# Performance work log

Hardware: AMD Instinct MI355X
Metric: run time of the kernel (lower is better)

## Reference

```python
import jax, jax.numpy as jnp
import numpy as np

B = 16384
K = 30
LAYERS = 3 * K          # 90
V_LEN = 2 * K           # 60
Z_LEN = 8 * K           # 240
IN_LEN = 3 * K + V_LEN  # 150


def setup_inputs() -> dict:
    key = jax.random.key(0)
    ks = jax.random.split(key, 9)
    Hr = jax.random.normal(ks[0], (B, K), dtype=jnp.float32)
    HH = jax.random.normal(ks[1], (B, K, K), dtype=jnp.float32)
    std = 0.01
    W1 = std * jax.random.normal(ks[2], (LAYERS, Z_LEN, IN_LEN), dtype=jnp.float32)
    b1 = std * jax.random.normal(ks[3], (LAYERS, Z_LEN), dtype=jnp.float32)
    W2 = std * jax.random.normal(ks[4], (LAYERS, K, Z_LEN), dtype=jnp.float32)
    b2 = std * jax.random.normal(ks[5], (LAYERS, K), dtype=jnp.float32)
    W3 = std * jax.random.normal(ks[6], (LAYERS, V_LEN, Z_LEN), dtype=jnp.float32)
    b3 = std * jax.random.normal(ks[7], (LAYERS, V_LEN), dtype=jnp.float32)
    kappa = jax.random.uniform(ks[8], (LAYERS,), dtype=jnp.float32)  # torch.rand(1) per layer
    return {"Hr": Hr, "HH": HH, "W1": W1, "b1": b1, "W2": W2, "b2": b2,
            "W3": W3, "b3": b3, "kappa": kappa}


def reference(Hr, HH, W1, b1, W2, b2, W3, b3, kappa):
    b = Hr.shape[0]
    v0 = jnp.zeros((b, V_LEN), dtype=Hr.dtype)
    t0 = jnp.zeros((b, K), dtype=Hr.dtype)
    tt0 = jnp.zeros((b, K), dtype=Hr.dtype)

    def step(carry, params):
        v, t, t_tilde = carry
        w1, bb1, w2, bb2, w3, bb3, kap = params
        tH = jnp.einsum('bk,bkj->bj', t, HH)                  # [B,K]
        concat = jnp.concatenate([Hr, v, t, tH], axis=1)      # [B,150]
        z = jax.nn.relu(concat @ w1.T + bb1)                  # [B,240]
        t_tilde = t_tilde + z @ w2.T + bb2                    # [B,30]
        ak = jnp.abs(kap)
        t_new = -1.0 + jax.nn.relu(t_tilde + kap) / ak - jax.nn.relu(t_tilde - kap) / ak
        v = v + z @ w3.T + bb3                                # [B,60]
        return (v, t_new, t_tilde), t_new

    _, ts = jax.lax.scan(step, (v0, t0, tt0), (W1, b1, W2, b2, W3, b3, kappa))
    return ts  # [LAYERS, B, K] == t[1:] in torch code
```

## Files before the change

kernel.cpp:

```cpp
#include <hip/hip_runtime.h>

typedef unsigned short u16;
typedef float    f32x4  __attribute__((ext_vector_type(4)));
typedef _Float16 f16x8  __attribute__((ext_vector_type(8)));
typedef short    short8 __attribute__((ext_vector_type(8)));

#define BB 16384
#define KK 30
#define NLAYER 90
#define ROWS 64
#define NBLK (BB / ROWS)
#define THREADS 1024

#define NT1 16
#define KS1 5
#define NT2 6
#define KS2 8

#define SZ1  (NLAYER * NT1 * KS1 * 512)
#define SZ23 (NLAYER * NT2 * KS2 * 512)
#define WS_NEEDED ((size_t)4 * (SZ1 + SZ23) + (size_t)4 * (NLAYER * 256 + NLAYER * 96))

#define A_STRIDE 168
#define Z_STRIDE 264
#define TO_STRIDE 33

#define MFMA(a, b, c) __builtin_amdgcn_mfma_f32_16x16x32_f16((a), (b), (c), 0, 0, 0)

__device__ __forceinline__ void splitf(float x, u16& hi, u16& lo) {
    _Float16 h = (_Float16)x;
    _Float16 l = (_Float16)(x - (float)h);
    hi = __builtin_bit_cast(u16, h);
    lo = __builtin_bit_cast(u16, l);
}
__device__ __forceinline__ f16x8 ldfrag(const u16* p) {
    return __builtin_bit_cast(f16x8, *(const short8*)p);
}

__global__ void prep(const float* __restrict__ W1, const float* __restrict__ W2,
                     const float* __restrict__ W3, const float* __restrict__ b1,
                     const float* __restrict__ b2, const float* __restrict__ b3,
                     u16* __restrict__ W1Fhi, u16* __restrict__ W1Flo,
                     u16* __restrict__ W23Fhi, u16* __restrict__ W23Flo,
                     float* __restrict__ b1p, float* __restrict__ b23p)
{
    int idx = blockIdx.x * 256 + threadIdx.x;
    if (idx < SZ1) {
        int j = idx & 7, lane = (idx >> 3) & 63;
        int r = idx >> 9, ks = r % 5; r /= 5;
        int nt = r % 16, l = r / 16;
        int k = ks * 32 + (lane >> 4) * 8 + j;
        int n = nt * 16 + (lane & 15);
        float wv = (k < 150 && n < 240) ? W1[((size_t)l * 240 + n) * 150 + k] : 0.f;
        splitf(wv, W1Fhi[idx], W1Flo[idx]);
    }
    if (idx < SZ23) {
        int j = idx & 7, lane = (idx >> 3) & 63;
        int r = idx >> 9, ks = r % 8; r /= 8;
        int nt = r % 6, l = r / 6;
        int k = ks * 32 + (lane >> 4) * 8 + j;
        int n = nt * 16 + (lane & 15);
        float wv = 0.f;
        if (k < 240) {
            if (n < 30)      wv = W2[((size_t)l * 30 + n) * 240 + k];
            else if (n < 90) wv = W3[((size_t)l * 60 + (n - 30)) * 240 + k];
        }
        splitf(wv, W23Fhi[idx], W23Flo[idx]);
    }
    if (idx < NLAYER * 256) {
        int l = idx >> 8, c = idx & 255;
        b1p[idx] = (c < 240) ? b1[l * 240 + c] : 0.f;
    }
    if (idx < NLAYER * 96) {
        int l = idx / 96, c = idx % 96;
        b23p[idx] = (c < 30) ? b2[l * 30 + c] : (c < 90 ? b3[l * 60 + (c - 30)] : 0.f);
    }
}

__global__ __launch_bounds__(THREADS, 4)
void detnet_kernel(const float* __restrict__ Hr, const float* __restrict__ HH,
                   const float* __restrict__ kappa,
                   const u16* __restrict__ W1Fhi, const u16* __restrict__ W1Flo,
                   const u16* __restrict__ W23Fhi, const u16* __restrict__ W23Flo,
                   const float* __restrict__ b1p, const float* __restrict__ b23p,
                   float* __restrict__ out)
{
    __shared__ u16 aT_hi[ROWS][A_STRIDE], aT_lo[ROWS][A_STRIDE];
    __shared__ u16 zT_hi[ROWS][Z_STRIDE], zT_lo[ROWS][Z_STRIDE];
    __shared__ float tOut[ROWS][TO_STRIDE];

    const int tid  = threadIdx.x;
    const int b0   = blockIdx.x * ROWS;
    const int w    = tid >> 6;
    const int lane = tid & 63;
    const int h    = lane >> 4;
    const int q    = lane & 15;

    const int ra = tid >> 4;
    const int sa = tid & 15;
    float2 hreg[KK];
    if (sa < 15) {
        const float* hh = HH + (size_t)(b0 + ra) * (KK * KK) + 2 * sa;
        #pragma unroll
        for (int k = 0; k < KK; ++k) hreg[k] = *(const float2*)(hh + k * KK);
    } else {
        #pragma unroll
        for (int k = 0; k < KK; ++k) hreg[k] = make_float2(0.f, 0.f);
    }

    const int cnt = w >> 1;
    const int cmh = w & 1;
    float st[2][4];
    #pragma unroll
    for (int m = 0; m < 2; ++m)
        #pragma unroll
        for (int r = 0; r < 4; ++r) st[m][r] = 0.f;

    for (int i = tid; i < ROWS * A_STRIDE; i += THREADS) { (&aT_hi[0][0])[i] = 0; (&aT_lo[0][0])[i] = 0; }
    for (int i = tid; i < ROWS * Z_STRIDE; i += THREADS) { (&zT_hi[0][0])[i] = 0; (&zT_lo[0][0])[i] = 0; }
    for (int i = tid; i < ROWS * TO_STRIDE; i += THREADS) (&tOut[0][0])[i] = 0.f;
    __syncthreads();
    for (int i = tid; i < ROWS * KK; i += THREADS) {
        int r = i / KK, k = i - r * KK;
        splitf(Hr[(size_t)(b0 + r) * KK + k], aT_hi[r][k], aT_lo[r][k]);
    }
    __syncthreads();

    for (int l = 0; l < NLAYER; ++l) {
        if (l > 0 && tid < ROWS * KK / 4) {
            f32x4 o;
            int e = tid * 4;
            #pragma unroll
            for (int i = 0; i < 4; ++i) {
                int ee = e + i, r = ee / 30, k2 = ee - 30 * r;
                o[i] = tOut[r][k2];
            }
            __builtin_nontemporal_store(o, (f32x4*)(out + ((size_t)(l - 1) * BB + b0) * KK + e));
        }

        if (l > 0 && sa < 15) {
            float a0 = 0.f, a1 = 0.f;
            #pragma unroll
            for (int k = 0; k < KK; ++k) {
                float tk = tOut[ra][k];
                a0 += tk * hreg[k].x;
                a1 += tk * hreg[k].y;
            }
            u16 h0, l0, h1, l1;
            splitf(a0, h0, l0); splitf(a1, h1, l1);
            *(unsigned int*)&aT_hi[ra][120 + 2 * sa] = (unsigned int)h0 | ((unsigned int)h1 << 16);
            *(unsigned int*)&aT_lo[ra][120 + 2 * sa] = (unsigned int)l0 | ((unsigned int)l1 << 16);
        }
        __syncthreads();

        {
            f32x4 acc[4];
            {
                float bi = b1p[l * 256 + w * 16 + q];
                f32x4 bv = {bi, bi, bi, bi};
                #pragma unroll
                for (int m = 0; m < 4; ++m) acc[m] = bv;
            }
            #pragma unroll 2
            for (int ks = 0; ks < KS1; ++ks) {
                size_t off = ((((size_t)l * NT1 + w) * KS1 + ks) * 64 + lane) * 8;
                f16x8 bh = ldfrag(W1Fhi + off);
                f16x8 bl = ldfrag(W1Flo + off);
                #pragma unroll
                for (int m = 0; m < 4; ++m) {
                    f16x8 ah = ldfrag(&aT_hi[m * 16 + q][ks * 32 + h * 8]);
                    f16x8 al = ldfrag(&aT_lo[m * 16 + q][ks * 32 + h * 8]);
                    acc[m] = MFMA(ah, bh, acc[m]);
                    acc[m] = MFMA(ah, bl, acc[m]);
                    acc[m] = MFMA(al, bh, acc[m]);
                }
            }
            #pragma unroll
            for (int m = 0; m < 4; ++m) {
                int col = w * 16 + q;
                #pragma unroll
                for (int reg = 0; reg < 4; ++reg) {
                    int row = m * 16 + 4 * h + reg;
                    float zv = fmaxf(acc[m][reg], 0.f);
                    splitf(zv, zT_hi[row][col], zT_lo[row][col]);
                }
            }
        }
        __syncthreads();

        if (w < 12) {
            const float kap = kappa[l];
            const float inv = 1.0f / fabsf(kap);
            f32x4 acc[2];
            {
                float bi = b23p[l * 96 + cnt * 16 + q];
                f32x4 bv = {bi, bi, bi, bi};
                acc[0] = bv; acc[1] = bv;
            }
            #pragma unroll 2
            for (int ks = 0; ks < KS2; ++ks) {
                size_t off = ((((size_t)l * NT2 + cnt) * KS2 + ks) * 64 + lane) * 8;
                f16x8 bh = ldfrag(W23Fhi + off);
                f16x8 bl = ldfrag(W23Flo + off);
                #pragma unroll
                for (int mm = 0; mm < 2; ++mm) {
                    f16x8 ah = ldfrag(&zT_hi[(cmh * 2 + mm) * 16 + q][ks * 32 + h * 8]);
                    f16x8 al = ldfrag(&zT_lo[(cmh * 2 + mm) * 16 + q][ks * 32 + h * 8]);
                    acc[mm] = MFMA(ah, bh, acc[mm]);
                    acc[mm] = MFMA(ah, bl, acc[mm]);
                    acc[mm] = MFMA(al, bh, acc[mm]);
                }
            }
            const int col = cnt * 16 + q;
            const bool isT = col < 30;
            const bool isV = (col >= 30) & (col < 90);
            #pragma unroll
            for (int mm = 0; mm < 2; ++mm)
                #pragma unroll
                for (int reg = 0; reg < 4; ++reg) {
                    float s2 = st[mm][reg] + acc[mm][reg];
                    int row = (cmh * 2 + mm) * 16 + 4 * h + reg;
                    if (isT) {
                        st[mm][reg] = s2;
                        float tn = -1.0f + fmaxf(s2 + kap, 0.f) * inv - fmaxf(s2 - kap, 0.f) * inv;
                        tOut[row][col] = tn;
                        splitf(tn, aT_hi[row][90 + col], aT_lo[row][90 + col]);
                    } else if (isV) {
                        st[mm][reg] = s2;
                        splitf(s2, aT_hi[row][col], aT_lo[row][col]);
                    }
                }
        }
        __syncthreads();
    }

    if (tid < ROWS * KK / 4) {
        f32x4 o;
        int e = tid * 4;
        #pragma unroll
        for (int i = 0; i < 4; ++i) {
            int ee = e + i, r = ee / 30, k2 = ee - 30 * r;
            o[i] = tOut[r][k2];
        }
        __builtin_nontemporal_store(o, (f32x4*)(out + ((size_t)(NLAYER - 1) * BB + b0) * KK + e));
    }
}

extern "C" void kernel_launch(void* const* d_in, const int* in_sizes, int n_in,
                              void* d_out, int out_size, void* d_ws, size_t ws_size,
                              hipStream_t stream) {
    const float* Hr = (const float*)d_in[0];
    const float* HH = (const float*)d_in[1];
    const float* W1 = (const float*)d_in[2];
    const float* b1 = (const float*)d_in[3];
    const float* W2 = (const float*)d_in[4];
    const float* b2 = (const float*)d_in[5];
    const float* W3 = (const float*)d_in[6];
    const float* b3 = (const float*)d_in[7];
    const float* kp = (const float*)d_in[8];
    float* out = (float*)d_out;

    if (ws_size < WS_NEEDED) return;

    u16* W1Fhi  = (u16*)d_ws;
    u16* W1Flo  = W1Fhi + SZ1;
    u16* W23Fhi = W1Flo + SZ1;
    u16* W23Flo = W23Fhi + SZ23;
    float* b1p  = (float*)(W23Flo + SZ23);
    float* b23p = b1p + NLAYER * 256;

    prep<<<dim3((SZ1 + 255) / 256), dim3(256), 0, stream>>>(
        W1, W2, W3, b1, b2, b3, W1Fhi, W1Flo, W23Fhi, W23Flo, b1p, b23p);
    detnet_kernel<<<dim3(NBLK), dim3(THREADS), 0, stream>>>(
        Hr, HH, kp, W1Fhi, W1Flo, W23Fhi, W23Flo, b1p, b23p, out);
}
```

Baseline: 759.2 us.

## Use 32x32x16 MFMA tiles for the first-layer GEMM

```diff
diff --git a/kernel.cpp b/kernel.cpp
--- a/kernel.cpp
+++ b/kernel.cpp
@@ -2,6 +2,7 @@
 
 typedef unsigned short u16;
 typedef float    f32x4  __attribute__((ext_vector_type(4)));
+typedef float    f32x16 __attribute__((ext_vector_type(16)));
 typedef _Float16 f16x8  __attribute__((ext_vector_type(8)));
 typedef short    short8 __attribute__((ext_vector_type(8)));
 
@@ -12,8 +13,8 @@
 #define NBLK (BB / ROWS)
 #define THREADS 1024
 
-#define NT1 16
-#define KS1 5
+#define NT1 8
+#define KS1 10
 #define NT2 6
 #define KS2 8
 
@@ -25,7 +26,8 @@
 #define Z_STRIDE 264
 #define TO_STRIDE 33
 
-#define MFMA(a, b, c) __builtin_amdgcn_mfma_f32_16x16x32_f16((a), (b), (c), 0, 0, 0)
+#define MFMA16(a, b, c) __builtin_amdgcn_mfma_f32_16x16x32_f16((a), (b), (c), 0, 0, 0)
+#define MFMA32(a, b, c) __builtin_amdgcn_mfma_f32_32x32x16_f16((a), (b), (c), 0, 0, 0)
 
 __device__ __forceinline__ void splitf(float x, u16& hi, u16& lo) {
     _Float16 h = (_Float16)x;
@@ -47,10 +49,10 @@
     int idx = blockIdx.x * 256 + threadIdx.x;
     if (idx < SZ1) {
         int j = idx & 7, lane = (idx >> 3) & 63;
-        int r = idx >> 9, ks = r % 5; r /= 5;
-        int nt = r % 16, l = r / 16;
-        int k = ks * 32 + (lane >> 4) * 8 + j;
-        int n = nt * 16 + (lane & 15);
+        int r = idx >> 9, ks = r % 10; r /= 10;
+        int nt = r % 8, l = r / 8;
+        int k = ks * 16 + (lane >> 5) * 8 + j;
+        int n = nt * 32 + (lane & 31);
         float wv = (k < 150 && n < 240) ? W1[((size_t)l * 240 + n) * 150 + k] : 0.f;
         splitf(wv, W1Fhi[idx], W1Flo[idx]);
     }
@@ -95,6 +97,14 @@
     const int lane = tid & 63;
     const int h    = lane >> 4;
     const int q    = lane & 15;
+    const int e31  = lane & 31;
+    const int e2   = lane >> 5;
+
+    const int nt8 = w & 7;
+    const int cmt = w >> 3;
+
+    const int cnt = w >> 1;
+    const int cmh = w & 1;
 
     const int ra = tid >> 4;
     const int sa = tid & 15;
@@ -108,8 +118,6 @@
         for (int k = 0; k < KK; ++k) hreg[k] = make_float2(0.f, 0.f);
     }
 
-    const int cnt = w >> 1;
-    const int cmh = w & 1;
     float st[2][4];
     #pragma unroll
     for (int m = 0; m < 2; ++m)
@@ -154,36 +162,29 @@
         __syncthreads();
 
         {
-            f32x4 acc[4];
+            f32x16 acc;
             {
-                float bi = b1p[l * 256 + w * 16 + q];
-                f32x4 bv = {bi, bi, bi, bi};
+                float bi = b1p[l * 256 + nt8 * 32 + e31];
                 #pragma unroll
-                for (int m = 0; m < 4; ++m) acc[m] = bv;
+                for (int r = 0; r < 16; ++r) acc[r] = bi;
             }
             #pragma unroll 2
             for (int ks = 0; ks < KS1; ++ks) {
-                size_t off = ((((size_t)l * NT1 + w) * KS1 + ks) * 64 + lane) * 8;
+                f16x8 ah = ldfrag(&aT_hi[cmt * 32 + e31][ks * 16 + e2 * 8]);
+                f16x8 al = ldfrag(&aT_lo[cmt * 32 + e31][ks * 16 + e2 * 8]);
+                size_t off = ((((size_t)l * NT1 + nt8) * KS1 + ks) * 64 + lane) * 8;
                 f16x8 bh = ldfrag(W1Fhi + off);
                 f16x8 bl = ldfrag(W1Flo + off);
-                #pragma unroll
-                for (int m = 0; m < 4; ++m) {
-                    f16x8 ah = ldfrag(&aT_hi[m * 16 + q][ks * 32 + h * 8]);
-                    f16x8 al = ldfrag(&aT_lo[m * 16 + q][ks * 32 + h * 8]);
-                    acc[m] = MFMA(ah, bh, acc[m]);
-                    acc[m] = MFMA(ah, bl, acc[m]);
-                    acc[m] = MFMA(al, bh, acc[m]);
-                }
-            }
-            #pragma unroll
-            for (int m = 0; m < 4; ++m) {
-                int col = w * 16 + q;
-                #pragma unroll
-                for (int reg = 0; reg < 4; ++reg) {
-                    int row = m * 16 + 4 * h + reg;
-                    float zv = fmaxf(acc[m][reg], 0.f);
-                    splitf(zv, zT_hi[row][col], zT_lo[row][col]);
-                }
+                acc = MFMA32(ah, bh, acc);
+                acc = MFMA32(ah, bl, acc);
+                acc = MFMA32(al, bh, acc);
+            }
+            const int col = nt8 * 32 + e31;
+            #pragma unroll
+            for (int reg = 0; reg < 16; ++reg) {
+                int row = cmt * 32 + (reg & 3) + 8 * (reg >> 2) + 4 * e2;
+                float zv = fmaxf(acc[reg], 0.f);
+                splitf(zv, zT_hi[row][col], zT_lo[row][col]);
             }
         }
         __syncthreads();
@@ -206,9 +207,9 @@
                 for (int mm = 0; mm < 2; ++mm) {
                     f16x8 ah = ldfrag(&zT_hi[(cmh * 2 + mm) * 16 + q][ks * 32 + h * 8]);
                     f16x8 al = ldfrag(&zT_lo[(cmh * 2 + mm) * 16 + q][ks * 32 + h * 8]);
-                    acc[mm] = MFMA(ah, bh, acc[mm]);
-                    acc[mm] = MFMA(ah, bl, acc[mm]);
-                    acc[mm] = MFMA(al, bh, acc[mm]);
+                    acc[mm] = MFMA16(ah, bh, acc[mm]);
+                    acc[mm] = MFMA16(ah, bl, acc[mm]);
+                    acc[mm] = MFMA16(al, bh, acc[mm]);
                 }
             }
             const int col = cnt * 16 + q;
```

New measurement: 914.6 us. 1.2x slower.

## Swap MFMA operands so outputs are row-contiguous and pad activation columns to multiples of 32

Applied to the files above, without the earlier changes.

```diff
diff --git a/kernel.cpp b/kernel.cpp
--- a/kernel.cpp
+++ b/kernel.cpp
@@ -4,6 +4,7 @@
 typedef float    f32x4  __attribute__((ext_vector_type(4)));
 typedef _Float16 f16x8  __attribute__((ext_vector_type(8)));
 typedef short    short8 __attribute__((ext_vector_type(8)));
+typedef unsigned short u16x4 __attribute__((ext_vector_type(4)));
 
 #define BB 16384
 #define KK 30
@@ -23,9 +24,9 @@
 
 #define A_STRIDE 168
 #define Z_STRIDE 264
-#define TO_STRIDE 33
-
-#define MFMA(a, b, c) __builtin_amdgcn_mfma_f32_16x16x32_f16((a), (b), (c), 0, 0, 0)
+#define TO_STRIDE 36
+
+#define MFMA16(a, b, c) __builtin_amdgcn_mfma_f32_16x16x32_f16((a), (b), (c), 0, 0, 0)
 
 __device__ __forceinline__ void splitf(float x, u16& hi, u16& lo) {
     _Float16 h = (_Float16)x;
@@ -49,9 +50,18 @@
         int j = idx & 7, lane = (idx >> 3) & 63;
         int r = idx >> 9, ks = r % 5; r /= 5;
         int nt = r % 16, l = r / 16;
-        int k = ks * 32 + (lane >> 4) * 8 + j;
-        int n = nt * 16 + (lane & 15);
-        float wv = (k < 150 && n < 240) ? W1[((size_t)l * 240 + n) * 150 + k] : 0.f;
+        int kc = ks * 32 + (lane >> 4) * 8 + j;
+        int n  = nt * 16 + (lane & 15);
+        float wv = 0.f;
+        if (n < 240) {
+            int k = -1;
+            if      (kc < 30)               k = kc;
+            else if (kc >= 32 && kc < 92)   k = kc - 2;
+            else if (kc >= 96 && kc < 126)  k = kc - 66 + 60 + 30 - 24;
+            else if (kc >= 128 && kc < 158) k = kc - 8;
+            if (kc >= 96 && kc < 126) k = kc - 6;
+            if (k >= 0) wv = W1[((size_t)l * 240 + n) * 150 + k];
+        }
         splitf(wv, W1Fhi[idx], W1Flo[idx]);
     }
     if (idx < SZ23) {
@@ -62,8 +72,8 @@
         int n = nt * 16 + (lane & 15);
         float wv = 0.f;
         if (k < 240) {
-            if (n < 30)      wv = W2[((size_t)l * 30 + n) * 240 + k];
-            else if (n < 90) wv = W3[((size_t)l * 60 + (n - 30)) * 240 + k];
+            if (n < 30)                wv = W2[((size_t)l * 30 + n) * 240 + k];
+            else if (n >= 32 && n < 92) wv = W3[((size_t)l * 60 + (n - 32)) * 240 + k];
         }
         splitf(wv, W23Fhi[idx], W23Flo[idx]);
     }
@@ -73,7 +83,8 @@
     }
     if (idx < NLAYER * 96) {
         int l = idx / 96, c = idx % 96;
-        b23p[idx] = (c < 30) ? b2[l * 30 + c] : (c < 90 ? b3[l * 60 + (c - 30)] : 0.f);
+        b23p[idx] = (c < 30) ? b2[l * 30 + c]
+                  : ((c >= 32 && c < 92) ? b3[l * 60 + (c - 32)] : 0.f);
     }
 }
 
@@ -96,6 +107,9 @@
     const int h    = lane >> 4;
     const int q    = lane & 15;
 
+    const int cnt = w >> 1;
+    const int cmh = w & 1;
+
     const int ra = tid >> 4;
     const int sa = tid & 15;
     float2 hreg[KK];
@@ -108,8 +122,6 @@
         for (int k = 0; k < KK; ++k) hreg[k] = make_float2(0.f, 0.f);
     }
 
-    const int cnt = w >> 1;
-    const int cmh = w & 1;
     float st[2][4];
     #pragma unroll
     for (int m = 0; m < 2; ++m)
@@ -148,42 +160,43 @@
             }
             u16 h0, l0, h1, l1;
             splitf(a0, h0, l0); splitf(a1, h1, l1);
-            *(unsigned int*)&aT_hi[ra][120 + 2 * sa] = (unsigned int)h0 | ((unsigned int)h1 << 16);
-            *(unsigned int*)&aT_lo[ra][120 + 2 * sa] = (unsigned int)l0 | ((unsigned int)l1 << 16);
+            *(unsigned int*)&aT_hi[ra][128 + 2 * sa] = (unsigned int)h0 | ((unsigned int)h1 << 16);
+            *(unsigned int*)&aT_lo[ra][128 + 2 * sa] = (unsigned int)l0 | ((unsigned int)l1 << 16);
         }
         __syncthreads();
 
         {
             f32x4 acc[4];
             {
-                float bi = b1p[l * 256 + w * 16 + q];
-                f32x4 bv = {bi, bi, bi, bi};
+                f32x4 bb = *(const f32x4*)&b1p[l * 256 + w * 16 + 4 * h];
                 #pragma unroll
-                for (int m = 0; m < 4; ++m) acc[m] = bv;
+                for (int m = 0; m < 4; ++m) acc[m] = bb;
             }
             #pragma unroll 2
             for (int ks = 0; ks < KS1; ++ks) {
                 size_t off = ((((size_t)l * NT1 + w) * KS1 + ks) * 64 + lane) * 8;
-                f16x8 bh = ldfrag(W1Fhi + off);
-                f16x8 bl = ldfrag(W1Flo + off);
+                f16x8 wh = ldfrag(W1Fhi + off);
+                f16x8 wl = ldfrag(W1Flo + off);
                 #pragma unroll
                 for (int m = 0; m < 4; ++m) {
                     f16x8 ah = ldfrag(&aT_hi[m * 16 + q][ks * 32 + h * 8]);
                     f16x8 al = ldfrag(&aT_lo[m * 16 + q][ks * 32 + h * 8]);
-                    acc[m] = MFMA(ah, bh, acc[m]);
-                    acc[m] = MFMA(ah, bl, acc[m]);
-                    acc[m] = MFMA(al, bh, acc[m]);
+                    acc[m] = MFMA16(wh, ah, acc[m]);
+                    acc[m] = MFMA16(wl, ah, acc[m]);
+                    acc[m] = MFMA16(wh, al, acc[m]);
                 }
             }
             #pragma unroll
             for (int m = 0; m < 4; ++m) {
-                int col = w * 16 + q;
+                u16x4 zh, zl;
                 #pragma unroll
                 for (int reg = 0; reg < 4; ++reg) {
-                    int row = m * 16 + 4 * h + reg;
                     float zv = fmaxf(acc[m][reg], 0.f);
-                    splitf(zv, zT_hi[row][col], zT_lo[row][col]);
+                    u16 a, b; splitf(zv, a, b);
+                    zh[reg] = a; zl[reg] = b;
                 }
+                *(u16x4*)&zT_hi[m * 16 + q][w * 16 + 4 * h] = zh;
+                *(u16x4*)&zT_lo[m * 16 + q][w * 16 + 4 * h] = zl;
             }
         }
         __syncthreads();
@@ -193,43 +206,64 @@
             const float inv = 1.0f / fabsf(kap);
             f32x4 acc[2];
             {
-                float bi = b23p[l * 96 + cnt * 16 + q];
-                f32x4 bv = {bi, bi, bi, bi};
-                acc[0] = bv; acc[1] = bv;
+                f32x4 bb = *(const f32x4*)&b23p[l * 96 + cnt * 16 + 4 * h];
+                acc[0] = bb; acc[1] = bb;
             }
             #pragma unroll 2
             for (int ks = 0; ks < KS2; ++ks) {
                 size_t off = ((((size_t)l * NT2 + cnt) * KS2 + ks) * 64 + lane) * 8;
-                f16x8 bh = ldfrag(W23Fhi + off);
-                f16x8 bl = ldfrag(W23Flo + off);
+                f16x8 wh = ldfrag(W23Fhi + off);
+                f16x8 wl = ldfrag(W23Flo + off);
                 #pragma unroll
                 for (int mm = 0; mm < 2; ++mm) {
-                    f16x8 ah = ldfrag(&zT_hi[(cmh * 2 + mm) * 16 + q][ks * 32 + h * 8]);
-                    f16x8 al = ldfrag(&zT_lo[(cmh * 2 + mm) * 16 + q][ks * 32 + h * 8]);
-                    acc[mm] = MFMA(ah, bh, acc[mm]);
-                    acc[mm] = MFMA(ah, bl, acc[mm]);
-                    acc[mm] = MFMA(al, bh, acc[mm]);
+                    f16x8 zh = ldfrag(&zT_hi[(cmh * 2 + mm) * 16 + q][ks * 32 + h * 8]);
+                    f16x8 zl = ldfrag(&zT_lo[(cmh * 2 + mm) * 16 + q][ks * 32 + h * 8]);
+                    acc[mm] = MFMA16(wh, zh, acc[mm]);
+                    acc[mm] = MFMA16(wl, zh, acc[mm]);
+                    acc[mm] = MFMA16(wh, zl, acc[mm]);
                 }
             }
-            const int col = cnt * 16 + q;
-            const bool isT = col < 30;
-            const bool isV = (col >= 30) & (col < 90);
+            const int nbase = cnt * 16 + 4 * h;
             #pragma unroll
-            for (int mm = 0; mm < 2; ++mm)
-                #pragma unroll
-                for (int reg = 0; reg < 4; ++reg) {
-                    float s2 = st[mm][reg] + acc[mm][reg];
-                    int row = (cmh * 2 + mm) * 16 + 4 * h + reg;
-                    if (isT) {
+            for (int mm = 0; mm < 2; ++mm) {
+                const int brow = (cmh * 2 + mm) * 16 + q;
+                if (nbase + 3 < 30) {
+                    f32x4 tn4;
+                    u16x4 th, tl;
+                    #pragma unroll
+                    for (int reg = 0; reg < 4; ++reg) {
+                        float s2 = st[mm][reg] + acc[mm][reg];
                         st[mm][reg] = s2;
                         float tn = -1.0f + fmaxf(s2 + kap, 0.f) * inv - fmaxf(s2 - kap, 0.f) * inv;
-                        tOut[row][col] = tn;
-                        splitf(tn, aT_hi[row][90 + col], aT_lo[row][90 + col]);
-                    } else if (isV) {
+                        tn4[reg] = tn;
+                        u16 a, b; splitf(tn, a, b);
+                        th[reg] = a; tl[reg] = b;
+                    }
+                    *(f32x4*)&tOut[brow][nbase] = tn4;
+                    *(u16x4*)&aT_hi[brow][96 + nbase] = th;
+                    *(u16x4*)&aT_lo[brow][96 + nbase] = tl;
+                } else if (nbase < 30) {
+                    #pragma unroll
+                    for (int reg = 0; reg < 2; ++reg) {
+                        float s2 = st[mm][reg] + acc[mm][reg];
                         st[mm][reg] = s2;
-                        splitf(s2, aT_hi[row][col], aT_lo[row][col]);
+                        float tn = -1.0f + fmaxf(s2 + kap, 0.f) * inv - fmaxf(s2 - kap, 0.f) * inv;
+                        tOut[brow][nbase + reg] = tn;
+                        splitf(tn, aT_hi[brow][96 + nbase + reg], aT_lo[brow][96 + nbase + reg]);
                     }
+                } else if (nbase >= 32 && nbase + 3 < 92) {
+                    u16x4 vh, vl;
+                    #pragma unroll
+                    for (int reg = 0; reg < 4; ++reg) {
+                        float s2 = st[mm][reg] + acc[mm][reg];
+                        st[mm][reg] = s2;
+                        u16 a, b; splitf(s2, a, b);
+                        vh[reg] = a; vl[reg] = b;
+                    }
+                    *(u16x4*)&aT_hi[brow][nbase] = vh;
+                    *(u16x4*)&aT_lo[brow][nbase] = vl;
                 }
+            }
         }
         __syncthreads();
     }
```

New measurement: 711.9 us. 1.07x faster.
